# Optimization experiments

Hardware: AMD Instinct MI355X
Metric: run time of the kernel (lower is better)

Reference implementation:

```python
import jax, jax.numpy as jnp
import numpy as np
import math

L = 12      # n_layer (alternating adaptive True/False)
H = 8       # n_head
C = 256     # n_embd
DH = C // H # head dim = 32
BS = 828    # block_size
T = 827     # seq len after dropping last token
VOCAB = 16384
CAM = 30
IMG = 256


def get_sinusoid(n_position, d_hid):
    pos = np.arange(n_position)[:, None].astype(np.float64)
    hid = np.arange(d_hid)[None, :]
    angle = pos / np.power(10000.0, 2.0 * (hid // 2) / d_hid)
    table = np.zeros_like(angle)
    table[:, 0::2] = np.sin(angle[:, 0::2])
    table[:, 1::2] = np.cos(angle[:, 1::2])
    return jnp.asarray(table[None], jnp.float32)  # [1, n_position, d_hid]


def layer_norm(x, w, b):
    m = x.mean(-1, keepdims=True)
    v = ((x - m) ** 2).mean(-1, keepdims=True)
    return (x - m) * jax.lax.rsqrt(v + 1e-5) * w + b


def setup_inputs() -> dict:
    key = jax.random.key(0)
    ks = iter(jax.random.split(key, 64))
    nrm = lambda shape, s=1.0: jax.random.normal(next(ks), shape, jnp.float32) * s
    B = 4
    inp = {
        'dc_emb': nrm((B, 572, C)),
        'z_emb': nrm((B, 256, C)),
        'p1': nrm((B, CAM)),
        'p2': nrm((B, CAM)),
        'p3': nrm((B, CAM)),
        'frame_emb': nrm((1, 256, C), 0.02),
        'camera_emb': nrm((1, 30, C), 0.02),
        'time_emb': get_sinusoid(BS, C),
        'loc_W1': nrm((2 * CAM, CAM), 0.02), 'loc_b1': jnp.zeros((2 * CAM,)),
        'loc_W2': nrm((IMG * IMG, 2 * CAM), 0.02), 'loc_b2': jnp.zeros((IMG * IMG,)),
        'ln1_w': jnp.ones((L, C)), 'ln1_b': jnp.zeros((L, C)),
        'Wq': nrm((L, C, C), 0.02), 'bq': jnp.zeros((L, C)),
        'Wk': nrm((L, C, C), 0.02), 'bk': jnp.zeros((L, C)),
        'Wv': nrm((L, C, C), 0.02), 'bv': jnp.zeros((L, C)),
        'Wo': nrm((L, C, C), 0.02), 'bo': jnp.zeros((L, C)),
        'ln2_w': jnp.ones((L, C)), 'ln2_b': jnp.zeros((L, C)),
        'W1': nrm((L, 4 * C, C), 0.02), 'b1': jnp.zeros((L, 4 * C)),
        'W2': nrm((L, C, 4 * C), 0.02), 'b2': jnp.zeros((L, C)),
        'lnf_w': jnp.ones((C,)), 'lnf_b': jnp.zeros((C,)),
        'head_W': nrm((VOCAB, C), 0.02),
    }
    return inp


def _forward(dc_emb, z_emb, p1, p2, p3, frame_emb, camera_emb, time_emb,
             loc_W1, loc_b1, loc_W2, loc_b2,
             ln1_w, ln1_b, Wq, bq, Wk, bk, Wv, bv, Wo, bo,
             ln2_w, ln2_b, W1, b1, W2, b2, lnf_w, lnf_b, head_W):
    B = dc_emb.shape[0]
    scale = 1.0 / math.sqrt(DH)

    # AdaptiveAttention bias h: [B, 1, BS, BS] with three 256x256 learned blocks
    def locality(p):
        z = jax.nn.gelu(p @ loc_W1.T + loc_b1, approximate=False)
        z = z @ loc_W2.T + loc_b2
        return z.reshape(B, IMG, IMG)

    h = jnp.zeros((B, 1, BS, BS), dc_emb.dtype)
    h = h.at[:, 0, 285:541, 0:256].set(locality(p1))
    h = h.at[:, 0, 571:827, 0:256].set(locality(p2))
    h = h.at[:, 0, 571:827, 286:542].set(locality(p3))
    h = h[:, :, :T, :T]

    # token + role + time embeddings
    tok = jnp.concatenate([dc_emb, z_emb], axis=1)[:, :-1, :]  # [B, T, C]
    role = jnp.concatenate([frame_emb, camera_emb, frame_emb, camera_emb, frame_emb], axis=1)[:, :T, :]
    x = tok + role + time_emb[:, :T, :]

    causal = jnp.tril(jnp.ones((T, T), bool))  # [T, T]

    for i in range(L):
        adaptive = (i % 2 == 0)
        xn = layer_norm(x, ln1_w[i], ln1_b[i])
        q = (xn @ Wq[i].T + bq[i]).reshape(B, T, H, DH)
        k = (xn @ Wk[i].T + bk[i]).reshape(B, T, H, DH)
        v = (xn @ Wv[i].T + bv[i]).reshape(B, T, H, DH)
        att = jnp.einsum('bqhd,bkhd->bhqk', q, k) * scale
        if adaptive:
            att = att + h
        att = jnp.where(causal, att, -jnp.inf)
        att = jax.nn.softmax(att, axis=-1)
        y = jnp.einsum('bhqk,bkhd->bqhd', att, v).reshape(B, T, C)
        x = x + y @ Wo[i].T + bo[i]
        xn2 = layer_norm(x, ln2_w[i], ln2_b[i])
        x = x + jax.nn.gelu(xn2 @ W1[i].T + b1[i], approximate=False) @ W2[i].T + b2[i]

    x = layer_norm(x, lnf_w, lnf_b)
    logits = x @ head_W.T  # [B, T, VOCAB]
    return logits


def reference(dc_emb, z_emb, p1, p2, p3, frame_emb, camera_emb, time_emb,
              loc_W1, loc_b1, loc_W2, loc_b2,
              ln1_w, ln1_b, Wq, bq, Wk, bk, Wv, bv, Wo, bo,
              ln2_w, ln2_b, W1, b1, W2, b2, lnf_w, lnf_b, head_W):
    return _forward(dc_emb, z_emb, p1, p2, p3, frame_emb, camera_emb, time_emb,
                    loc_W1, loc_b1, loc_W2, loc_b2,
                    ln1_w, ln1_b, Wq, bq, Wk, bk, Wv, bv, Wo, bo,
                    ln2_w, ln2_b, W1, b1, W2, b2, lnf_w, lnf_b, head_W)
```

## Files before the change

kernel.cpp:

```cpp
#include <hip/hip_runtime.h>
#include <hip/hip_bf16.h>
#include <math.h>

#define T_LEN 827
#define M_ROWS 3308
#define NLAYER 12

typedef __attribute__((ext_vector_type(4))) float f32x4;
typedef __attribute__((ext_vector_type(8))) short bf16x8;

__device__ __forceinline__ float gelu_f(float x) {
    return 0.5f * x * (1.0f + erff(x * 0.70710678118654752440f));
}

__device__ __forceinline__ short f2bf_s(float x) {
    __hip_bfloat16 h = __float2bfloat16(x);
    return *reinterpret_cast<short*>(&h);
}

__global__ void cvt_kernel(const float* __restrict__ in, __hip_bfloat16* __restrict__ out, int n4) {
    int i = blockIdx.x * blockDim.x + threadIdx.x;
    if (i >= n4) return;
    float4 v = reinterpret_cast<const float4*>(in)[i];
    out[4*i+0] = __float2bfloat16(v.x);
    out[4*i+1] = __float2bfloat16(v.y);
    out[4*i+2] = __float2bfloat16(v.z);
    out[4*i+3] = __float2bfloat16(v.w);
}

__global__ void prep_wqkv_kernel(const float* __restrict__ Wq, const float* __restrict__ Wk,
                                 const float* __restrict__ Wv, __hip_bfloat16* __restrict__ out) {
    int i = blockIdx.x * 256 + threadIdx.x;
    if (i >= 12*768*64) return;
    int el = i * 4;
    int layer = el / (768*256);
    int rem = el % (768*256);
    int row = rem >> 8, col = rem & 255;
    const float* src;
    float sc = 1.f;
    if (row < 256)      { src = Wq + ((size_t)layer*256 + row)*256 + col; sc = 0.17677669529663687f; }
    else if (row < 512) { src = Wk + ((size_t)layer*256 + (row-256))*256 + col; }
    else                { src = Wv + ((size_t)layer*256 + (row-512))*256 + col; }
    float4 v = *reinterpret_cast<const float4*>(src);
    out[el+0] = __float2bfloat16(v.x * sc);
    out[el+1] = __float2bfloat16(v.y * sc);
    out[el+2] = __float2bfloat16(v.z * sc);
    out[el+3] = __float2bfloat16(v.w * sc);
}

__global__ void prep_bqkv_kernel(const float* __restrict__ bq, const float* __restrict__ bk,
                                 const float* __restrict__ bv, float* __restrict__ out) {
    int i = blockIdx.x * 256 + threadIdx.x;
    if (i >= 12*768) return;
    int layer = i / 768, row = i % 768;
    float v;
    if (row < 256)      v = bq[layer*256 + row] * 0.17677669529663687f;
    else if (row < 512) v = bk[layer*256 + (row-256)];
    else                v = bv[layer*256 + (row-512)];
    out[i] = v;
}

__global__ void zero_kernel(float* __restrict__ p, int n) {
    for (int i = blockIdx.x * blockDim.x + threadIdx.x; i < n; i += gridDim.x * blockDim.x)
        p[i] = 0.f;
}

__global__ void loc_z1_kernel(const float* __restrict__ p1, const float* __restrict__ p2,
                              const float* __restrict__ p3, const float* __restrict__ W1,
                              const float* __restrict__ b1, float* __restrict__ z1) {
    for (int i = threadIdx.x; i < 720; i += 256) {
        int pi = i / 240, rem = i % 240, b = rem / 60, j = rem % 60;
        const float* p = (pi == 0) ? p1 : ((pi == 1) ? p2 : p3);
        float acc = b1[j];
        #pragma unroll
        for (int c = 0; c < 30; ++c) acc += p[b*30 + c] * W1[j*30 + c];
        z1[i] = gelu_f(acc);
    }
}

__global__ void h_fill_kernel(const float* __restrict__ z1, const float* __restrict__ W2,
                              const float* __restrict__ b2, __hip_bfloat16* __restrict__ h) {
    __shared__ float z[720];
    int tid = threadIdx.x;
    for (int i = tid; i < 720; i += 256) z[i] = z1[i];
    __syncthreads();
    int j = blockIdx.x * 256 + tid;
    float w[60];
    #pragma unroll
    for (int c = 0; c < 60; ++c) w[c] = W2[(size_t)j*60 + c];
    float bj = b2[j];
    int r = j >> 8, cc = j & 255;
    const int br[3] = {285, 571, 571};
    const int bc[3] = {0, 0, 286};
    #pragma unroll
    for (int pi = 0; pi < 3; ++pi) {
        for (int b = 0; b < 4; ++b) {
            float acc = bj;
            #pragma unroll
            for (int c = 0; c < 60; ++c) acc += z[pi*240 + b*60 + c] * w[c];
            h[(size_t)b*T_LEN*T_LEN + (size_t)(br[pi] + r)*T_LEN + bc[pi] + cc] = __float2bfloat16(acc);
        }
    }
}

__global__ void init_x_kernel(const float* __restrict__ dc, const float* __restrict__ z,
                              const float* __restrict__ frame, const float* __restrict__ cam,
                              const float* __restrict__ timeE, float* __restrict__ x) {
    int idx = blockIdx.x * 256 + threadIdx.x;
    int m = idx >> 8, c = idx & 255;
    int b = m / T_LEN, t = m % T_LEN;
    float tok = (t < 572) ? dc[((size_t)b*572 + t)*256 + c]
                          : z[((size_t)b*256 + (t - 572))*256 + c];
    float role;
    if      (t < 256) role = frame[t*256 + c];
    else if (t < 286) role = cam[(t-256)*256 + c];
    else if (t < 542) role = frame[(t-286)*256 + c];
    else if (t < 572) role = cam[(t-542)*256 + c];
    else              role = frame[(t-572)*256 + c];
    x[idx] = tok + role + timeE[t*256 + c];
}

__global__ __launch_bounds__(256) void ln_kernel(const float* __restrict__ x,
                                                 const float* __restrict__ w,
                                                 const float* __restrict__ b,
                                                 __hip_bfloat16* __restrict__ out) {
    int row = blockIdx.x, tid = threadIdx.x;
    float v = x[(size_t)row*256 + tid];
    float s = v;
    #pragma unroll
    for (int off = 32; off; off >>= 1) s += __shfl_down(s, off);
    __shared__ float red[4];
    if ((tid & 63) == 0) red[tid >> 6] = s;
    __syncthreads();
    float mean = (red[0] + red[1] + red[2] + red[3]) * (1.f/256.f);
    float d = v - mean;
    float s2 = d * d;
    #pragma unroll
    for (int off = 32; off; off >>= 1) s2 += __shfl_down(s2, off);
    __shared__ float red2[4];
    if ((tid & 63) == 0) red2[tid >> 6] = s2;
    __syncthreads();
    float var = (red2[0] + red2[1] + red2[2] + red2[3]) * (1.f/256.f);
    float rs = rsqrtf(var + 1e-5f);
    out[(size_t)row*256 + tid] = __float2bfloat16(d * rs * w[tid] + b[tid]);
}

template<bool LN, bool RESID, bool OUTBF16>
__global__ __launch_bounds__(256) void gemm_k256(
    const float* __restrict__ xsrc, const float* __restrict__ lnw, const float* __restrict__ lnb,
    const __hip_bfloat16* __restrict__ Abf,
    const __hip_bfloat16* __restrict__ W, const float* __restrict__ bias,
    const float* __restrict__ resid, void* __restrict__ out, int M, int N)
{
    __shared__ __hip_bfloat16 As[64][264];
    __shared__ __hip_bfloat16 Bs[64][264];
    __shared__ float redS[4][64], redQ[4][64];
    const int tid = threadIdx.x;
    const int m0 = blockIdx.x * 64, n0 = blockIdx.y * 64;
    const int r = tid >> 2, sg = tid & 3;

    {
        const __hip_bfloat16* bsrc = W + (size_t)(n0 + r) * 256 + sg * 8;
        #pragma unroll
        for (int j = 0; j < 8; ++j)
            *reinterpret_cast<uint4*>(&Bs[r][sg*8 + j*32]) =
                *reinterpret_cast<const uint4*>(bsrc + j*32);
    }
    int gr = m0 + r; if (gr > M-1) gr = M-1;
    if constexpr (LN) {
        const float* src = xsrc + (size_t)gr * 256;
        float s = 0.f, q = 0.f;
        #pragma unroll
        for (int j = 0; j < 8; ++j) {
            int k = sg*8 + j*32;
            float4 a = *reinterpret_cast<const float4*>(src + k);
            float4 c4 = *reinterpret_cast<const float4*>(src + k + 4);
            s += a.x + a.y + a.z + a.w + c4.x + c4.y + c4.z + c4.w;
            q += a.x*a.x + a.y*a.y + a.z*a.z + a.w*a.w
               + c4.x*c4.x + c4.y*c4.y + c4.z*c4.z + c4.w*c4.w;
        }
        redS[sg][r] = s; redQ[sg][r] = q;
        __syncthreads();
        float mean = (redS[0][r] + redS[1][r] + redS[2][r] + redS[3][r]) * (1.f/256.f);
        float msq  = (redQ[0][r] + redQ[1][r] + redQ[2][r] + redQ[3][r]) * (1.f/256.f);
        float rstd = rsqrtf(msq - mean*mean + 1e-5f);
        #pragma unroll
        for (int j = 0; j < 8; ++j) {
            int k = sg*8 + j*32;
            float4 a = *reinterpret_cast<const float4*>(src + k);
            float4 c4 = *reinterpret_cast<const float4*>(src + k + 4);
            float v[8] = {a.x, a.y, a.z, a.w, c4.x, c4.y, c4.z, c4.w};
            bf16x8 pk;
            #pragma unroll
            for (int e = 0; e < 8; ++e)
                pk[e] = f2bf_s((v[e] - mean) * rstd * lnw[k+e] + lnb[k+e]);
            *reinterpret_cast<bf16x8*>(&As[r][k]) = pk;
        }
    } else {
        const __hip_bfloat16* asrc = Abf + (size_t)gr * 256 + sg * 8;
        #pragma unroll
        for (int j = 0; j < 8; ++j)
            *reinterpret_cast<uint4*>(&As[r][sg*8 + j*32]) =
                *reinterpret_cast<const uint4*>(asrc + j*32);
    }
    __syncthreads();

    const int wid = tid >> 6, lane = tid & 63;
    const int wm = wid >> 1, wn = wid & 1, c = lane & 15, g = lane >> 4;
    f32x4 acc[2][2];
    #pragma unroll
    for (int mi = 0; mi < 2; ++mi)
        #pragma unroll
        for (int ni = 0; ni < 2; ++ni)
            acc[mi][ni] = (f32x4){0.f, 0.f, 0.f, 0.f};

    #pragma unroll
    for (int kj = 0; kj < 8; ++kj) {
        bf16x8 a0 = *reinterpret_cast<const bf16x8*>(&As[wm*32 + c][kj*32 + g*8]);
        bf16x8 a1 = *reinterpret_cast<const bf16x8*>(&As[wm*32 + 16 + c][kj*32 + g*8]);
        bf16x8 b0 = *reinterpret_cast<const bf16x8*>(&Bs[wn*32 + c][kj*32 + g*8]);
        bf16x8 b1v = *reinterpret_cast<const bf16x8*>(&Bs[wn*32 + 16 + c][kj*32 + g*8]);
        acc[0][0] = __builtin_amdgcn_mfma_f32_16x16x32_bf16(a0, b0, acc[0][0], 0, 0, 0);
        acc[0][1] = __builtin_amdgcn_mfma_f32_16x16x32_bf16(a0, b1v, acc[0][1], 0, 0, 0);
        acc[1][0] = __builtin_amdgcn_mfma_f32_16x16x32_bf16(a1, b0, acc[1][0], 0, 0, 0);
        acc[1][1] = __builtin_amdgcn_mfma_f32_16x16x32_bf16(a1, b1v, acc[1][1], 0, 0, 0);
    }

    #pragma unroll
    for (int mi = 0; mi < 2; ++mi) {
        #pragma unroll
        for (int ni = 0; ni < 2; ++ni) {
            int n = n0 + wn*32 + ni*16 + c;
            float bb = bias ? bias[n] : 0.f;
            #pragma unroll
            for (int rg = 0; rg < 4; ++rg) {
                int m = m0 + wm*32 + mi*16 + g*4 + rg;
                if (m >= M) continue;
                float v = acc[mi][ni][rg] + bb;
                if (RESID) v += resid[(size_t)m*N + n];
                if (OUTBF16) ((__hip_bfloat16*)out)[(size_t)m*N + n] = __float2bfloat16(v);
                else         ((float*)out)[(size_t)m*N + n] = v;
            }
        }
    }
}

__global__ __launch_bounds__(512) void mlp_fused(
    float* __restrict__ x,
    const float* __restrict__ ln2w, const float* __restrict__ ln2b,
    const __hip_bfloat16* __restrict__ W1, const float* __restrict__ b1,
    const __hip_bfloat16* __restrict__ W2, const float* __restrict__ b2,
    const float* __restrict__ lnow, const float* __restrict__ lnob,
    __hip_bfloat16* __restrict__ xn)
{
    __shared__ __hip_bfloat16 As[32][264];
    __shared__ __hip_bfloat16 Ms[32][1044];
    const int tid = threadIdx.x;
    const int m0 = blockIdx.x * 32;
    const int w = tid >> 6, lane = tid & 63, c = lane & 15, g = lane >> 4;

    {
        int r = tid >> 4, p = tid & 15;
        int gr = m0 + r; if (gr > M_ROWS-1) gr = M_ROWS-1;
        const float* src = x + (size_t)gr*256 + p*16;
        float4 f0 = *reinterpret_cast<const float4*>(src);
        float4 f1 = *reinterpret_cast<const float4*>(src + 4);
        float4 f2 = *reinterpret_cast<const float4*>(src + 8);
        float4 f3 = *reinterpret_cast<const float4*>(src + 12);
        float vv[16] = {f0.x,f0.y,f0.z,f0.w, f1.x,f1.y,f1.z,f1.w,
                        f2.x,f2.y,f2.z,f2.w, f3.x,f3.y,f3.z,f3.w};
        float s = 0.f, q = 0.f;
        #pragma unroll
        for (int e = 0; e < 16; ++e) { s += vv[e]; q += vv[e]*vv[e]; }
        #pragma unroll
        for (int msk = 1; msk <= 8; msk <<= 1) { s += __shfl_xor(s, msk); q += __shfl_xor(q, msk); }
        float mean = s * (1.f/256.f);
        float rstd = rsqrtf(q*(1.f/256.f) - mean*mean + 1e-5f);
        bf16x8 pk0, pk1;
        #pragma unroll
        for (int e = 0; e < 8; ++e) {
            pk0[e] = f2bf_s((vv[e]   - mean)*rstd*ln2w[p*16+e]   + ln2b[p*16+e]);
            pk1[e] = f2bf_s((vv[8+e] - mean)*rstd*ln2w[p*16+8+e] + ln2b[p*16+8+e]);
        }
        *reinterpret_cast<bf16x8*>(&As[r][p*16])     = pk0;
        *reinterpret_cast<bf16x8*>(&As[r][p*16 + 8]) = pk1;
    }
    __syncthreads();

    #pragma unroll 1
    for (int ns = 0; ns < 8; ++ns) {
        int nb = w*128 + ns*16;
        const __hip_bfloat16* wrow = W1 + (size_t)(nb + c)*256 + g*8;
        f32x4 a0 = (f32x4){0.f,0.f,0.f,0.f}, a1 = (f32x4){0.f,0.f,0.f,0.f};
        #pragma unroll
        for (int kj = 0; kj < 8; ++kj) {
            bf16x8 bfrag = *reinterpret_cast<const bf16x8*>(wrow + kj*32);
            bf16x8 af0 = *reinterpret_cast<const bf16x8*>(&As[c][kj*32 + g*8]);
            bf16x8 af1 = *reinterpret_cast<const bf16x8*>(&As[16 + c][kj*32 + g*8]);
            a0 = __builtin_amdgcn_mfma_f32_16x16x32_bf16(af0, bfrag, a0, 0, 0, 0);
            a1 = __builtin_amdgcn_mfma_f32_16x16x32_bf16(af1, bfrag, a1, 0, 0, 0);
        }
        float bb = b1[nb + c];
        #pragma unroll
        for (int rg = 0; rg < 4; ++rg) {
            Ms[g*4 + rg][nb + c]      = __float2bfloat16(gelu_f(a0[rg] + bb));
            Ms[16 + g*4 + rg][nb + c] = __float2bfloat16(gelu_f(a1[rg] + bb));
        }
    }
    __syncthreads();

    f32x4 o[2][2];
    #pragma unroll
    for (int i = 0; i < 2; ++i)
        #pragma unroll
        for (int j = 0; j < 2; ++j)
            o[i][j] = (f32x4){0.f,0.f,0.f,0.f};
    #pragma unroll
    for (int ns2 = 0; ns2 < 2; ++ns2) {
        int nb = w*32 + ns2*16;
        const __hip_bfloat16* wrow = W2 + (size_t)(nb + c)*1024 + g*8;
        #pragma unroll
        for (int kj = 0; kj < 32; ++kj) {
            bf16x8 bfrag = *reinterpret_cast<const bf16x8*>(wrow + kj*32);
            bf16x8 af0 = *reinterpret_cast<const bf16x8*>(&Ms[c][kj*32 + g*8]);
            bf16x8 af1 = *reinterpret_cast<const bf16x8*>(&Ms[16 + c][kj*32 + g*8]);
            o[ns2][0] = __builtin_amdgcn_mfma_f32_16x16x32_bf16(af0, bfrag, o[ns2][0], 0, 0, 0);
            o[ns2][1] = __builtin_amdgcn_mfma_f32_16x16x32_bf16(af1, bfrag, o[ns2][1], 0, 0, 0);
        }
    }
    __syncthreads();

    float* xf = reinterpret_cast<float*>(&Ms[0][0]);
    #pragma unroll
    for (int ns2 = 0; ns2 < 2; ++ns2) {
        int nb = w*32 + ns2*16;
        float bb = b2[nb + c];
        #pragma unroll
        for (int mi = 0; mi < 2; ++mi) {
            #pragma unroll
            for (int rg = 0; rg < 4; ++rg) {
                int row = mi*16 + g*4 + rg;
                int gm = m0 + row;
                if (gm < M_ROWS) {
                    float v = o[ns2][mi][rg] + bb + x[(size_t)gm*256 + nb + c];
                    x[(size_t)gm*256 + nb + c] = v;
                    xf[row*256 + nb + c] = v;
                }
            }
        }
    }
    __syncthreads();

    {
        int r = tid >> 4, p = tid & 15;
        int gm = m0 + r;
        const float* src = xf + r*256 + p*16;
        float4 f0 = *reinterpret_cast<const float4*>(src);
        float4 f1 = *reinterpret_cast<const float4*>(src + 4);
        float4 f2 = *reinterpret_cast<const float4*>(src + 8);
        float4 f3 = *reinterpret_cast<const float4*>(src + 12);
        float vv[16] = {f0.x,f0.y,f0.z,f0.w, f1.x,f1.y,f1.z,f1.w,
                        f2.x,f2.y,f2.z,f2.w, f3.x,f3.y,f3.z,f3.w};
        float s = 0.f, q = 0.f;
        #pragma unroll
        for (int e = 0; e < 16; ++e) { s += vv[e]; q += vv[e]*vv[e]; }
        #pragma unroll
        for (int msk = 1; msk <= 8; msk <<= 1) { s += __shfl_xor(s, msk); q += __shfl_xor(q, msk); }
        float mean = s * (1.f/256.f);
        float rstd = rsqrtf(q*(1.f/256.f) - mean*mean + 1e-5f);
        if (gm < M_ROWS) {
            bf16x8 pk0, pk1;
            #pragma unroll
            for (int e = 0; e < 8; ++e) {
                pk0[e] = f2bf_s((vv[e]   - mean)*rstd*lnow[p*16+e]   + lnob[p*16+e]);
                pk1[e] = f2bf_s((vv[8+e] - mean)*rstd*lnow[p*16+8+e] + lnob[p*16+8+e]);
            }
            *reinterpret_cast<bf16x8*>(&xn[(size_t)gm*256 + p*16])     = pk0;
            *reinterpret_cast<bf16x8*>(&xn[(size_t)gm*256 + p*16 + 8]) = pk1;
        }
    }
}

template<int ADAPT>
__global__ __launch_bounds__(256) void attn_split_kernel(const __hip_bfloat16* __restrict__ qkv,
                                                         const __hip_bfloat16* __restrict__ hbuf,
                                                         float* __restrict__ pacc,
                                                         float* __restrict__ pml) {
    const int fi = blockIdx.x, hh = blockIdx.y, b = blockIdx.z;
    int qi = 0;
    while (qi < 12) {
        int n1 = qi + 1;
        int bn = n1 + (n1 > 4 ? n1 - 4 : 0) + (n1 > 8 ? n1 - 8 : 0);
        if (fi < bn) break;
        ++qi;
    }
    const int base = qi + (qi > 4 ? qi - 4 : 0) + (qi > 8 ? qi - 8 : 0);
    const int ck = fi - base;
    const int q0 = qi * 64;
    const int kstart = ck * 256;
    const int kend = min(q0 + 64, T_LEN);
    const int nit = min(4, (kend - kstart + 63) >> 6);

    const int tid = threadIdx.x;
    const int w = tid >> 6, lane = tid & 63;
    const int c = lane & 15, g = lane >> 4;
    const int qw0 = q0 + w * 16;

    __shared__ short Ks[2][64][40];
    __shared__ short Vt[2][32][68];
    __shared__ short Pw[4][16][72];

    int qrow = qw0 + c; if (qrow > T_LEN-1) qrow = T_LEN-1;
    bf16x8 aq = *reinterpret_cast<const bf16x8*>(qkv + ((size_t)b*T_LEN + qrow)*768 + hh*32 + g*8);

    float m_r[4] = {-INFINITY, -INFINITY, -INFINITY, -INFINITY};
    float l_r[4] = {0.f, 0.f, 0.f, 0.f};
    f32x4 acc[2];
    acc[0] = (f32x4){0.f,0.f,0.f,0.f};
    acc[1] = (f32x4){0.f,0.f,0.f,0.f};

    const int srow = tid >> 2;
    const int scol8 = (tid & 3) * 8;

    bf16x8 kreg, vreg;
    {
        int krow = kstart + srow; if (krow > T_LEN-1) krow = T_LEN-1;
        const __hip_bfloat16* gbase = qkv + ((size_t)b*T_LEN + krow)*768 + hh*32 + scol8;
        kreg = *reinterpret_cast<const bf16x8*>(gbase + 256);
        vreg = *reinterpret_cast<const bf16x8*>(gbase + 512);
    }

    for (int it = 0; it < nit; ++it) {
        const int bsel = it & 1;
        const int kb = kstart + it * 64;
        *reinterpret_cast<bf16x8*>(&Ks[bsel][srow][scol8]) = kreg;
        #pragma unroll
        for (int jj = 0; jj < 8; ++jj) Vt[bsel][scol8 + jj][srow] = vreg[jj];
        __syncthreads();
        if (it + 1 < nit) {
            int krow = kb + 64 + srow; if (krow > T_LEN-1) krow = T_LEN-1;
            const __hip_bfloat16* gbase = qkv + ((size_t)b*T_LEN + krow)*768 + hh*32 + scol8;
            kreg = *reinterpret_cast<const bf16x8*>(gbase + 256);
            vreg = *reinterpret_cast<const bf16x8*>(gbase + 512);
        }

        f32x4 sc4[4];
        #pragma unroll
        for (int j = 0; j < 4; ++j) {
            bf16x8 bk = *reinterpret_cast<const bf16x8*>(&Ks[bsel][j*16 + c][g*8]);
            sc4[j] = __builtin_amdgcn_mfma_f32_16x16x32_bf16(aq, bk, (f32x4){0.f,0.f,0.f,0.f}, 0, 0, 0);
        }

        float sv[4][4];
        #pragma unroll
        for (int j = 0; j < 4; ++j) {
            int kk = kb + j*16 + c;
            #pragma unroll
            for (int rg = 0; rg < 4; ++rg) {
                int qq = qw0 + g*4 + rg;
                bool valid = (qq < T_LEN) && (kk <= qq);
                float s = sc4[j][rg];
                if (ADAPT) s += valid ? __bfloat162float(hbuf[((size_t)b*T_LEN + qq)*T_LEN + kk]) : 0.f;
                sv[j][rg] = valid ? s : -INFINITY;
            }
        }

        float sf[4];
        #pragma unroll
        for (int rg = 0; rg < 4; ++rg) {
            float m = fmaxf(fmaxf(sv[0][rg], sv[1][rg]), fmaxf(sv[2][rg], sv[3][rg]));
            #pragma unroll
            for (int msk = 1; msk <= 8; msk <<= 1) m = fmaxf(m, __shfl_xor(m, msk));
            float mn = fmaxf(m_r[rg], m);
            sf[rg] = __expf(m_r[rg] - mn);
            m_r[rg] = mn;
        }
        float p[4][4];
        #pragma unroll
        for (int rg = 0; rg < 4; ++rg) {
            float su = 0.f;
            #pragma unroll
            for (int j = 0; j < 4; ++j) {
                float e = __expf(sv[j][rg] - m_r[rg]);
                p[j][rg] = e;
                su += e;
            }
            #pragma unroll
            for (int msk = 1; msk <= 8; msk <<= 1) su += __shfl_xor(su, msk);
            l_r[rg] = l_r[rg] * sf[rg] + su;
            acc[0][rg] *= sf[rg];
            acc[1][rg] *= sf[rg];
        }

        #pragma unroll
        for (int j = 0; j < 4; ++j)
            #pragma unroll
            for (int rg = 0; rg < 4; ++rg)
                Pw[w][g*4 + rg][j*16 + c] = f2bf_s(p[j][rg]);

        #pragma unroll
        for (int kc = 0; kc < 2; ++kc) {
            bf16x8 ap = *reinterpret_cast<const bf16x8*>(&Pw[w][c][kc*32 + g*8]);
            #pragma unroll
            for (int dt = 0; dt < 2; ++dt) {
                bf16x8 bv = *reinterpret_cast<const bf16x8*>(&Vt[bsel][dt*16 + c][kc*32 + g*8]);
                acc[dt] = __builtin_amdgcn_mfma_f32_16x16x32_bf16(ap, bv, acc[dt], 0, 0, 0);
            }
        }
    }

    const int slot = (b*8 + hh)*28 + fi;
    float* paccs = pacc + (size_t)slot * 2048;
    #pragma unroll
    for (int rg = 0; rg < 4; ++rg) {
        int row = w*16 + g*4 + rg;
        paccs[row*32 + c]      = acc[0][rg];
        paccs[row*32 + 16 + c] = acc[1][rg];
        if (c == 0) {
            pml[(size_t)slot*128 + row*2]     = m_r[rg];
            pml[(size_t)slot*128 + row*2 + 1] = l_r[rg];
        }
    }
}

__global__ __launch_bounds__(256) void attn_merge_kernel(const float* __restrict__ pacc,
                                                         const float* __restrict__ pml,
                                                         __hip_bfloat16* __restrict__ y) {
    const int qi = blockIdx.x, hh = blockIdx.y, b = blockIdx.z;
    const int nc = qi/4 + 1;
    const int base = qi + (qi > 4 ? qi - 4 : 0) + (qi > 8 ? qi - 8 : 0);
    const int slot0 = (b*8 + hh)*28 + base;
    const int t = threadIdx.x, d = t & 31, r8 = t >> 5;
    for (int rr = r8; rr < 64; rr += 8) {
        int qq = qi*64 + rr;
        if (qq >= T_LEN) continue;
        float M = -INFINITY;
        for (int cc2 = 0; cc2 < nc; ++cc2)
            M = fmaxf(M, pml[(size_t)(slot0+cc2)*128 + rr*2]);
        float L = 0.f, o = 0.f;
        for (int cc2 = 0; cc2 < nc; ++cc2) {
            float mm = pml[(size_t)(slot0+cc2)*128 + rr*2];
            float ll = pml[(size_t)(slot0+cc2)*128 + rr*2 + 1];
            float sc = __expf(mm - M);
            L += sc * ll;
            o += sc * pacc[(size_t)(slot0+cc2)*2048 + rr*32 + d];
        }
        y[((size_t)b*T_LEN + qq)*256 + hh*32 + d] = __float2bfloat16(o / L);
    }
}

extern "C" void kernel_launch(void* const* d_in, const int* in_sizes, int n_in,
                              void* d_out, int out_size, void* d_ws, size_t ws_size,
                              hipStream_t stream) {
    const float* dc    = (const float*)d_in[0];
    const float* zemb  = (const float*)d_in[1];
    const float* p1    = (const float*)d_in[2];
    const float* p2    = (const float*)d_in[3];
    const float* p3    = (const float*)d_in[4];
    const float* frame = (const float*)d_in[5];
    const float* cam   = (const float*)d_in[6];
    const float* timeE = (const float*)d_in[7];
    const float* locW1 = (const float*)d_in[8];
    const float* locb1 = (const float*)d_in[9];
    const float* locW2 = (const float*)d_in[10];
    const float* locb2 = (const float*)d_in[11];
    const float* ln1w  = (const float*)d_in[12];
    const float* ln1b  = (const float*)d_in[13];
    const float* Wq    = (const float*)d_in[14];
    const float* bq    = (const float*)d_in[15];
    const float* Wk    = (const float*)d_in[16];
    const float* bk    = (const float*)d_in[17];
    const float* Wv    = (const float*)d_in[18];
    const float* bv    = (const float*)d_in[19];
    const float* Wo    = (const float*)d_in[20];
    const float* bo    = (const float*)d_in[21];
    const float* ln2w  = (const float*)d_in[22];
    const float* ln2b  = (const float*)d_in[23];
    const float* W1p   = (const float*)d_in[24];
    const float* b1p   = (const float*)d_in[25];
    const float* W2p   = (const float*)d_in[26];
    const float* b2p   = (const float*)d_in[27];
    const float* lnfw  = (const float*)d_in[28];
    const float* lnfb  = (const float*)d_in[29];
    const float* headW = (const float*)d_in[30];

    char* wsb = (char*)d_ws;
    size_t off = 0;
    auto alloc = [&](size_t bytes) -> char* {
        char* p = wsb + off;
        off += (bytes + 255) & ~(size_t)255;
        return p;
    };
    __hip_bfloat16* wqkv_bf = (__hip_bfloat16*)alloc(12ull*768*256*2);
    float*          bqkv    = (float*)alloc(12ull*768*4);
    __hip_bfloat16* wo_bf = (__hip_bfloat16*)alloc(12ull*65536*2);
    __hip_bfloat16* w1_bf = (__hip_bfloat16*)alloc(12ull*262144*2);
    __hip_bfloat16* w2_bf = (__hip_bfloat16*)alloc(12ull*262144*2);
    __hip_bfloat16* wh_bf = (__hip_bfloat16*)alloc(16384ull*256*2);
    __hip_bfloat16* hbuf = (__hip_bfloat16*)alloc(4ull*T_LEN*T_LEN*2);
    float* x    = (float*)alloc((size_t)M_ROWS*256*4);
    __hip_bfloat16* xn   = (__hip_bfloat16*)alloc((size_t)M_ROWS*256*2);
    __hip_bfloat16* qkvb = (__hip_bfloat16*)alloc((size_t)M_ROWS*768*2);
    __hip_bfloat16* yb   = (__hip_bfloat16*)alloc((size_t)M_ROWS*256*2);
    float* pacc = (float*)alloc(32ull*28*2048*4);
    float* pml  = (float*)alloc(32ull*28*128*4);
    float* z1   = (float*)alloc(720*4);

    prep_wqkv_kernel<<<(12*768*64 + 255)/256, 256, 0, stream>>>(Wq, Wk, Wv, wqkv_bf);
    prep_bqkv_kernel<<<36, 256, 0, stream>>>(bq, bk, bv, bqkv);
    cvt_kernel<<<768, 256, 0, stream>>>(Wo, wo_bf, 196608);
    cvt_kernel<<<3072, 256, 0, stream>>>(W1p, w1_bf, 786432);
    cvt_kernel<<<3072, 256, 0, stream>>>(W2p, w2_bf, 786432);
    cvt_kernel<<<4096, 256, 0, stream>>>(headW, wh_bf, 1048576);

    loc_z1_kernel<<<1, 256, 0, stream>>>(p1, p2, p3, locW1, locb1, z1);
    zero_kernel<<<2048, 256, 0, stream>>>((float*)hbuf, (4*T_LEN*T_LEN)/2);
    h_fill_kernel<<<256, 256, 0, stream>>>(z1, locW2, locb2, hbuf);

    init_x_kernel<<<M_ROWS, 256, 0, stream>>>(dc, zemb, frame, cam, timeE, x);
    ln_kernel<<<M_ROWS, 256, 0, stream>>>(x, ln1w, ln1b, xn);

    dim3 gqkv(52, 12);
    dim3 goproj(52, 4);
    dim3 gsplit(28, 8, 4);
    dim3 gmerge(13, 8, 4);

    for (int i = 0; i < NLAYER; ++i) {
        gemm_k256<false,false,true><<<gqkv, 256, 0, stream>>>(
            nullptr, nullptr, nullptr, xn,
            wqkv_bf + (size_t)i*196608, bqkv + i*768, nullptr, qkvb, M_ROWS, 768);
        if (i % 2 == 0) attn_split_kernel<1><<<gsplit, 256, 0, stream>>>(qkvb, hbuf, pacc, pml);
        else            attn_split_kernel<0><<<gsplit, 256, 0, stream>>>(qkvb, hbuf, pacc, pml);
        attn_merge_kernel<<<gmerge, 256, 0, stream>>>(pacc, pml, yb);
        gemm_k256<false,true,false><<<goproj, 256, 0, stream>>>(
            nullptr, nullptr, nullptr, yb,
            wo_bf + (size_t)i*65536, bo + i*256, x, x, M_ROWS, 256);
        const float* lnow = (i == NLAYER-1) ? lnfw : (ln1w + (i+1)*256);
        const float* lnob = (i == NLAYER-1) ? lnfb : (ln1b + (i+1)*256);
        mlp_fused<<<104, 512, 0, stream>>>(
            x, ln2w + i*256, ln2b + i*256,
            w1_bf + (size_t)i*262144, b1p + i*1024,
            w2_bf + (size_t)i*262144, b2p + i*256, lnow, lnob, xn);
    }

    gemm_k256<false,false,false><<<dim3(52, 256), 256, 0, stream>>>(
        nullptr, nullptr, nullptr, xn, wh_bf, nullptr, nullptr, (float*)d_out, M_ROWS, 16384);
}
```

Measured before the change: 1.354 ms.

## Fuse split-K attention and merge into one two-group in-block kernel

```diff
diff --git a/kernel.cpp b/kernel.cpp
--- a/kernel.cpp
+++ b/kernel.cpp
@@ -5,6 +5,7 @@
 #define T_LEN 827
 #define M_ROWS 3308
 #define NLAYER 12
+#define NEG_SENT -1e30f
 
 typedef __attribute__((ext_vector_type(4))) float f32x4;
 typedef __attribute__((ext_vector_type(8))) short bf16x8;
@@ -145,16 +146,14 @@
     out[(size_t)row*256 + tid] = __float2bfloat16(d * rs * w[tid] + b[tid]);
 }
 
-template<bool LN, bool RESID, bool OUTBF16>
+template<bool RESID, bool OUTBF16>
 __global__ __launch_bounds__(256) void gemm_k256(
-    const float* __restrict__ xsrc, const float* __restrict__ lnw, const float* __restrict__ lnb,
     const __hip_bfloat16* __restrict__ Abf,
     const __hip_bfloat16* __restrict__ W, const float* __restrict__ bias,
     const float* __restrict__ resid, void* __restrict__ out, int M, int N)
 {
     __shared__ __hip_bfloat16 As[64][264];
     __shared__ __hip_bfloat16 Bs[64][264];
-    __shared__ float redS[4][64], redQ[4][64];
     const int tid = threadIdx.x;
     const int m0 = blockIdx.x * 64, n0 = blockIdx.y * 64;
     const int r = tid >> 2, sg = tid & 3;
@@ -167,36 +166,7 @@
                 *reinterpret_cast<const uint4*>(bsrc + j*32);
     }
     int gr = m0 + r; if (gr > M-1) gr = M-1;
-    if constexpr (LN) {
-        const float* src = xsrc + (size_t)gr * 256;
-        float s = 0.f, q = 0.f;
-        #pragma unroll
-        for (int j = 0; j < 8; ++j) {
-            int k = sg*8 + j*32;
-            float4 a = *reinterpret_cast<const float4*>(src + k);
-            float4 c4 = *reinterpret_cast<const float4*>(src + k + 4);
-            s += a.x + a.y + a.z + a.w + c4.x + c4.y + c4.z + c4.w;
-            q += a.x*a.x + a.y*a.y + a.z*a.z + a.w*a.w
-               + c4.x*c4.x + c4.y*c4.y + c4.z*c4.z + c4.w*c4.w;
-        }
-        redS[sg][r] = s; redQ[sg][r] = q;
-        __syncthreads();
-        float mean = (redS[0][r] + redS[1][r] + redS[2][r] + redS[3][r]) * (1.f/256.f);
-        float msq  = (redQ[0][r] + redQ[1][r] + redQ[2][r] + redQ[3][r]) * (1.f/256.f);
-        float rstd = rsqrtf(msq - mean*mean + 1e-5f);
-        #pragma unroll
-        for (int j = 0; j < 8; ++j) {
-            int k = sg*8 + j*32;
-            float4 a = *reinterpret_cast<const float4*>(src + k);
-            float4 c4 = *reinterpret_cast<const float4*>(src + k + 4);
-            float v[8] = {a.x, a.y, a.z, a.w, c4.x, c4.y, c4.z, c4.w};
-            bf16x8 pk;
-            #pragma unroll
-            for (int e = 0; e < 8; ++e)
-                pk[e] = f2bf_s((v[e] - mean) * rstd * lnw[k+e] + lnb[k+e]);
-            *reinterpret_cast<bf16x8*>(&As[r][k]) = pk;
-        }
-    } else {
+    {
         const __hip_bfloat16* asrc = Abf + (size_t)gr * 256 + sg * 8;
         #pragma unroll
         for (int j = 0; j < 8; ++j)
@@ -382,72 +352,65 @@
 }
 
 template<int ADAPT>
-__global__ __launch_bounds__(256) void attn_split_kernel(const __hip_bfloat16* __restrict__ qkv,
-                                                         const __hip_bfloat16* __restrict__ hbuf,
-                                                         float* __restrict__ pacc,
-                                                         float* __restrict__ pml) {
-    const int fi = blockIdx.x, hh = blockIdx.y, b = blockIdx.z;
-    int qi = 0;
-    while (qi < 12) {
-        int n1 = qi + 1;
-        int bn = n1 + (n1 > 4 ? n1 - 4 : 0) + (n1 > 8 ? n1 - 8 : 0);
-        if (fi < bn) break;
-        ++qi;
-    }
-    const int base = qi + (qi > 4 ? qi - 4 : 0) + (qi > 8 ? qi - 8 : 0);
-    const int ck = fi - base;
-    const int q0 = qi * 64;
-    const int kstart = ck * 256;
-    const int kend = min(q0 + 64, T_LEN);
-    const int nit = min(4, (kend - kstart + 63) >> 6);
-
+__global__ __launch_bounds__(512) void attn_v3_kernel(const __hip_bfloat16* __restrict__ qkv,
+                                                      const __hip_bfloat16* __restrict__ hbuf,
+                                                      __hip_bfloat16* __restrict__ y) {
+    const int qi = blockIdx.x, hh = blockIdx.y, b = blockIdx.z;
     const int tid = threadIdx.x;
     const int w = tid >> 6, lane = tid & 63;
     const int c = lane & 15, g = lane >> 4;
-    const int qw0 = q0 + w * 16;
-
-    __shared__ short Ks[2][64][40];
-    __shared__ short Vt[2][32][68];
-    __shared__ short Pw[4][16][72];
+    const int qsub = w & 3, grp = w >> 2;
+    const int q0 = qi * 64;
+    const int qw0 = q0 + qsub * 16;
+    const int nt = qi + 1;
+    const int h = (nt + 1) >> 1;
+
+    __shared__ short Ks[2][2][64][40];
+    __shared__ short Vt[2][2][32][68];
+    __shared__ short Pw[8][16][72];
+    __shared__ float mlS[4][16][2];
 
     int qrow = qw0 + c; if (qrow > T_LEN-1) qrow = T_LEN-1;
     bf16x8 aq = *reinterpret_cast<const bf16x8*>(qkv + ((size_t)b*T_LEN + qrow)*768 + hh*32 + g*8);
 
-    float m_r[4] = {-INFINITY, -INFINITY, -INFINITY, -INFINITY};
+    float m_r[4] = {NEG_SENT, NEG_SENT, NEG_SENT, NEG_SENT};
     float l_r[4] = {0.f, 0.f, 0.f, 0.f};
     f32x4 acc[2];
     acc[0] = (f32x4){0.f,0.f,0.f,0.f};
     acc[1] = (f32x4){0.f,0.f,0.f,0.f};
 
-    const int srow = tid >> 2;
-    const int scol8 = (tid & 3) * 8;
+    const int lt = tid & 255;
+    const int srow = lt >> 2;
+    const int scol8 = (lt & 3) * 8;
 
     bf16x8 kreg, vreg;
     {
-        int krow = kstart + srow; if (krow > T_LEN-1) krow = T_LEN-1;
-        const __hip_bfloat16* gbase = qkv + ((size_t)b*T_LEN + krow)*768 + hh*32 + scol8;
-        kreg = *reinterpret_cast<const bf16x8*>(gbase + 256);
-        vreg = *reinterpret_cast<const bf16x8*>(gbase + 512);
-    }
-
-    for (int it = 0; it < nit; ++it) {
+        int kb0 = (grp ? h : 0) * 64;
+        int krow = kb0 + srow; if (krow > T_LEN-1) krow = T_LEN-1;
+        const __hip_bfloat16* gb = qkv + ((size_t)b*T_LEN + krow)*768 + hh*32 + scol8;
+        kreg = *reinterpret_cast<const bf16x8*>(gb + 256);
+        vreg = *reinterpret_cast<const bf16x8*>(gb + 512);
+    }
+
+    for (int it = 0; it < h; ++it) {
         const int bsel = it & 1;
-        const int kb = kstart + it * 64;
-        *reinterpret_cast<bf16x8*>(&Ks[bsel][srow][scol8]) = kreg;
-        #pragma unroll
-        for (int jj = 0; jj < 8; ++jj) Vt[bsel][scol8 + jj][srow] = vreg[jj];
+        const int kb = (grp ? h + it : it) * 64;
+        *reinterpret_cast<bf16x8*>(&Ks[grp][bsel][srow][scol8]) = kreg;
+        #pragma unroll
+        for (int jj = 0; jj < 8; ++jj) Vt[grp][bsel][scol8 + jj][srow] = vreg[jj];
         __syncthreads();
-        if (it + 1 < nit) {
-            int krow = kb + 64 + srow; if (krow > T_LEN-1) krow = T_LEN-1;
-            const __hip_bfloat16* gbase = qkv + ((size_t)b*T_LEN + krow)*768 + hh*32 + scol8;
-            kreg = *reinterpret_cast<const bf16x8*>(gbase + 256);
-            vreg = *reinterpret_cast<const bf16x8*>(gbase + 512);
+        if (it + 1 < h) {
+            int kbn = (grp ? h + it + 1 : it + 1) * 64;
+            int krow = kbn + srow; if (krow > T_LEN-1) krow = T_LEN-1;
+            const __hip_bfloat16* gb = qkv + ((size_t)b*T_LEN + krow)*768 + hh*32 + scol8;
+            kreg = *reinterpret_cast<const bf16x8*>(gb + 256);
+            vreg = *reinterpret_cast<const bf16x8*>(gb + 512);
         }
 
         f32x4 sc4[4];
         #pragma unroll
         for (int j = 0; j < 4; ++j) {
-            bf16x8 bk = *reinterpret_cast<const bf16x8*>(&Ks[bsel][j*16 + c][g*8]);
+            bf16x8 bk = *reinterpret_cast<const bf16x8*>(&Ks[grp][bsel][j*16 + c][g*8]);
             sc4[j] = __builtin_amdgcn_mfma_f32_16x16x32_bf16(aq, bk, (f32x4){0.f,0.f,0.f,0.f}, 0, 0, 0);
         }
 
@@ -461,7 +424,7 @@
                 bool valid = (qq < T_LEN) && (kk <= qq);
                 float s = sc4[j][rg];
                 if (ADAPT) s += valid ? __bfloat162float(hbuf[((size_t)b*T_LEN + qq)*T_LEN + kk]) : 0.f;
-                sv[j][rg] = valid ? s : -INFINITY;
+                sv[j][rg] = valid ? s : NEG_SENT;
             }
         }
 
@@ -503,49 +466,42 @@
             bf16x8 ap = *reinterpret_cast<const bf16x8*>(&Pw[w][c][kc*32 + g*8]);
             #pragma unroll
             for (int dt = 0; dt < 2; ++dt) {
-                bf16x8 bv = *reinterpret_cast<const bf16x8*>(&Vt[bsel][dt*16 + c][kc*32 + g*8]);
+                bf16x8 bv = *reinterpret_cast<const bf16x8*>(&Vt[grp][bsel][dt*16 + c][kc*32 + g*8]);
                 acc[dt] = __builtin_amdgcn_mfma_f32_16x16x32_bf16(ap, bv, acc[dt], 0, 0, 0);
             }
         }
     }
 
-    const int slot = (b*8 + hh)*28 + fi;
-    float* paccs = pacc + (size_t)slot * 2048;
-    #pragma unroll
-    for (int rg = 0; rg < 4; ++rg) {
-        int row = w*16 + g*4 + rg;
-        paccs[row*32 + c]      = acc[0][rg];
-        paccs[row*32 + 16 + c] = acc[1][rg];
-        if (c == 0) {
-            pml[(size_t)slot*128 + row*2]     = m_r[rg];
-            pml[(size_t)slot*128 + row*2 + 1] = l_r[rg];
-        }
-    }
-}
-
-__global__ __launch_bounds__(256) void attn_merge_kernel(const float* __restrict__ pacc,
-                                                         const float* __restrict__ pml,
-                                                         __hip_bfloat16* __restrict__ y) {
-    const int qi = blockIdx.x, hh = blockIdx.y, b = blockIdx.z;
-    const int nc = qi/4 + 1;
-    const int base = qi + (qi > 4 ? qi - 4 : 0) + (qi > 8 ? qi - 8 : 0);
-    const int slot0 = (b*8 + hh)*28 + base;
-    const int t = threadIdx.x, d = t & 31, r8 = t >> 5;
-    for (int rr = r8; rr < 64; rr += 8) {
-        int qq = qi*64 + rr;
-        if (qq >= T_LEN) continue;
-        float M = -INFINITY;
-        for (int cc2 = 0; cc2 < nc; ++cc2)
-            M = fmaxf(M, pml[(size_t)(slot0+cc2)*128 + rr*2]);
-        float L = 0.f, o = 0.f;
-        for (int cc2 = 0; cc2 < nc; ++cc2) {
-            float mm = pml[(size_t)(slot0+cc2)*128 + rr*2];
-            float ll = pml[(size_t)(slot0+cc2)*128 + rr*2 + 1];
-            float sc = __expf(mm - M);
-            L += sc * ll;
-            o += sc * pacc[(size_t)(slot0+cc2)*2048 + rr*32 + d];
-        }
-        y[((size_t)b*T_LEN + qq)*256 + hh*32 + d] = __float2bfloat16(o / L);
+    if (grp == 1) {
+        float* accS = reinterpret_cast<float*>(&Pw[4 + qsub][0][0]);
+        #pragma unroll
+        for (int rg = 0; rg < 4; ++rg) {
+            int row = g*4 + rg;
+            accS[row*32 + c]      = acc[0][rg];
+            accS[row*32 + 16 + c] = acc[1][rg];
+            if (c == 0) { mlS[qsub][row][0] = m_r[rg]; mlS[qsub][row][1] = l_r[rg]; }
+        }
+    }
+    __syncthreads();
+    if (grp == 0) {
+        const float* accS = reinterpret_cast<const float*>(&Pw[4 + qsub][0][0]);
+        #pragma unroll
+        for (int rg = 0; rg < 4; ++rg) {
+            int row = g*4 + rg;
+            int qq = qw0 + row;
+            if (qq >= T_LEN) continue;
+            float m1 = mlS[qsub][row][0], l1 = mlS[qsub][row][1];
+            float M = fmaxf(m_r[rg], m1);
+            float a = __expf(m_r[rg] - M);
+            float bsc = __expf(m1 - M);
+            float L = l_r[rg]*a + l1*bsc;
+            float inv = 1.f / L;
+            float o0 = (acc[0][rg]*a + accS[row*32 + c]*bsc) * inv;
+            float o1 = (acc[1][rg]*a + accS[row*32 + 16 + c]*bsc) * inv;
+            size_t yo = ((size_t)b*T_LEN + qq)*256 + hh*32;
+            y[yo + c]      = __float2bfloat16(o0);
+            y[yo + 16 + c] = __float2bfloat16(o1);
+        }
     }
 }
 
@@ -602,8 +558,6 @@
     __hip_bfloat16* xn   = (__hip_bfloat16*)alloc((size_t)M_ROWS*256*2);
     __hip_bfloat16* qkvb = (__hip_bfloat16*)alloc((size_t)M_ROWS*768*2);
     __hip_bfloat16* yb   = (__hip_bfloat16*)alloc((size_t)M_ROWS*256*2);
-    float* pacc = (float*)alloc(32ull*28*2048*4);
-    float* pml  = (float*)alloc(32ull*28*128*4);
     float* z1   = (float*)alloc(720*4);
 
     prep_wqkv_kernel<<<(12*768*64 + 255)/256, 256, 0, stream>>>(Wq, Wk, Wv, wqkv_bf);
@@ -622,19 +576,15 @@
 
     dim3 gqkv(52, 12);
     dim3 goproj(52, 4);
-    dim3 gsplit(28, 8, 4);
-    dim3 gmerge(13, 8, 4);
+    dim3 gattn(13, 8, 4);
 
     for (int i = 0; i < NLAYER; ++i) {
-        gemm_k256<false,false,true><<<gqkv, 256, 0, stream>>>(
-            nullptr, nullptr, nullptr, xn,
-            wqkv_bf + (size_t)i*196608, bqkv + i*768, nullptr, qkvb, M_ROWS, 768);
-        if (i % 2 == 0) attn_split_kernel<1><<<gsplit, 256, 0, stream>>>(qkvb, hbuf, pacc, pml);
-        else            attn_split_kernel<0><<<gsplit, 256, 0, stream>>>(qkvb, hbuf, pacc, pml);
-        attn_merge_kernel<<<gmerge, 256, 0, stream>>>(pacc, pml, yb);
-        gemm_k256<false,true,false><<<goproj, 256, 0, stream>>>(
-            nullptr, nullptr, nullptr, yb,
-            wo_bf + (size_t)i*65536, bo + i*256, x, x, M_ROWS, 256);
+        gemm_k256<false,true><<<gqkv, 256, 0, stream>>>(
+            xn, wqkv_bf + (size_t)i*196608, bqkv + i*768, nullptr, qkvb, M_ROWS, 768);
+        if (i % 2 == 0) attn_v3_kernel<1><<<gattn, 512, 0, stream>>>(qkvb, hbuf, yb);
+        else            attn_v3_kernel<0><<<gattn, 512, 0, stream>>>(qkvb, hbuf, yb);
+        gemm_k256<true,false><<<goproj, 256, 0, stream>>>(
+            yb, wo_bf + (size_t)i*65536, bo + i*256, x, x, M_ROWS, 256);
         const float* lnow = (i == NLAYER-1) ? lnfw : (ln1w + (i+1)*256);
         const float* lnob = (i == NLAYER-1) ? lnfb : (ln1b + (i+1)*256);
         mlp_fused<<<104, 512, 0, stream>>>(
@@ -643,6 +593,6 @@
             w2_bf + (size_t)i*262144, b2p + i*256, lnow, lnob, xn);
     }
 
-    gemm_k256<false,false,false><<<dim3(52, 256), 256, 0, stream>>>(
-        nullptr, nullptr, nullptr, xn, wh_bf, nullptr, nullptr, (float*)d_out, M_ROWS, 16384);
-}
+    gemm_k256<false,false><<<dim3(52, 256), 256, 0, stream>>>(
+        xn, wh_bf, nullptr, nullptr, (float*)d_out, M_ROWS, 16384);
+}
```

New measurement: 1.249 ms. -7.8%, faster.
